# Optimization experiments

Measured on AMD Instinct MI355X. Metric: run time of the kernel, lower is better.

## Reference

```python
import jax, jax.numpy as jnp
import numpy as np


def _greedy_nms_single(scores, suppress):
    """Greedy score-ordered suppression for one scene.
    scores: [P] float max class score; suppress: [P, P] bool, row i suppresses col j
    (same class AND within class radius of point i). Returns keep mask [P] bool."""
    P = scores.shape[0]

    def cond(state):
        alive, _ = state
        return jnp.any(alive)

    def body(state):
        alive, keep = state
        i = jnp.argmax(jnp.where(alive, scores, -jnp.inf))  # highest-score remaining
        keep = keep.at[i].set(True)
        alive = alive & ~suppress[i]   # drop same-class points within radius of i
        alive = alive.at[i].set(False)
        return alive, keep

    alive0 = jnp.ones((P,), dtype=bool)
    keep0 = jnp.zeros((P,), dtype=bool)
    _, keep = jax.lax.while_loop(cond, body, (alive0, keep0))
    return keep


def _keep_mask(centers, cls_preds, class_radius):
    # centers: [B,P,3], cls_preds: [B,P,K], class_radius: [K]
    scores = jnp.max(cls_preds, axis=-1)     # [B,P]  torch.max(..., dim=1) values
    labels = jnp.argmax(cls_preds, axis=-1)  # [B,P]  torch.max(..., dim=1) indices
    diff = centers[:, :, None, :] - centers[:, None, :, :]        # [B,P,P,3]
    dist = jnp.sqrt(jnp.sum(diff * diff, axis=-1))                # [B,P,P] torch.norm
    same_class = labels[:, :, None] == labels[:, None, :]         # [B,P,P]
    radii = class_radius[labels]                                  # [B,P] radius of keeper i
    suppress = same_class & (dist < radii[:, :, None])            # [B,P,P]
    return jax.vmap(_greedy_nms_single)(scores, suppress)         # [B,P] bool


def setup_inputs() -> dict:
    key = jax.random.key(0)
    k1, k2, k3, k4 = jax.random.split(key, 4)
    B, P, C, K = 8, 2048, 1024, 3
    centers = jax.random.normal(k1, (B, P, 3), dtype=jnp.float32)
    features = jax.random.normal(k2, (B, P, C), dtype=jnp.float32)
    cls_preds = jax.random.normal(k3, (B, P, K), dtype=jnp.float32)
    class_radius = jax.random.uniform(k4, (K,), dtype=jnp.float32)  # per-class NMS radius
    return {"centers": centers, "features": features, "cls_preds": cls_preds,
            "class_radius": class_radius}


def reference(centers, features, cls_preds, class_radius):
    """Greedy per-class radius-based keypoint suppression (fixed-shape variant):
    instead of dynamically gathering kept points (data-dependent shape), we return
    the boolean keep mask and the inputs with suppressed entries zeroed out."""
    keep = _keep_mask(centers, cls_preds, class_radius)      # [B,P] bool
    m = keep[..., None].astype(features.dtype)
    return (centers * m, features * m, cls_preds * m, keep)
```

## Files before the change

kernel.cpp:

```cpp
#include <hip/hip_runtime.h>

#define B 8
#define P 2048
#define C 1024
#define NCHUNK 32
#define FEAT4 (B*P*C/4)
#define CEN4  (B*P*3/4)

typedef unsigned long long u64;
typedef unsigned int u32;

__global__ __launch_bounds__(512) void rank_kernel(
    const float* __restrict__ centers,
    const float* __restrict__ cls_preds,
    float4* __restrict__ scent,
    int* __restrict__ sidx)
{
    __shared__ u64 s_keys[P];
    __shared__ u32 s_cnt[64][9];
    const int b = blockIdx.x >> 5, gi = blockIdx.x & 31;
    const int tid = threadIdx.x, wv = tid >> 6, lane = tid & 63;
    const float* clsb = cls_preds + (size_t)b * P * 3;
    const float* cenb = centers + (size_t)b * P * 3;

    for (int e = tid; e < P; e += 512) {
        float s0 = clsb[e*3], s1 = clsb[e*3+1], s2 = clsb[e*3+2];
        float sc = s0; int lb = 0;
        if (s1 > sc) { sc = s1; lb = 1; }
        if (s2 > sc) { sc = s2; lb = 2; }
        u32 ub = __float_as_uint(sc);
        u32 ord = (ub & 0x80000000u) ? ~ub : (ub | 0x80000000u);
        s_keys[e] = ((u64)(~ord) << 32) | (u32)((e << 2) | lb);
    }
    __syncthreads();

    const u64 myk = s_keys[(gi << 6) + lane];
    u32 c = 0;
    const int sbase = wv << 8;
    #pragma unroll 8
    for (int u = 0; u < 256; ++u)
        c += (s_keys[sbase + u] < myk) ? 1u : 0u;
    s_cnt[lane][wv] = c;
    __syncthreads();

    if (wv == 0) {
        u32 rank = 0;
        #pragma unroll
        for (int s = 0; s < 8; ++s) rank += s_cnt[lane][s];
        u32 lo = (u32)myk;
        int orig = (int)(lo >> 2);
        float4 cc;
        cc.x = cenb[orig*3]; cc.y = cenb[orig*3+1]; cc.z = cenb[orig*3+2];
        cc.w = __int_as_float((int)(lo & 3));
        scent[(size_t)b * P + rank] = cc;
        sidx[(size_t)b * P + rank] = (int)lo;
    }
}

__global__ __launch_bounds__(512) void matrix_kernel(
    const float4* __restrict__ scent,
    const float* __restrict__ class_radius,
    u32* __restrict__ matT)
{
    __shared__ float4 s_cent[P];
    const int b = blockIdx.x >> 5, gi = blockIdx.x & 31;
    const int tid = threadIdx.x, wv = tid >> 6, lane = tid & 63;

    const float4 cj = scent[(size_t)b * P + (gi << 6) + lane];
    const int labj = __float_as_int(cj.w);
    const float r = class_radius[labj];
    const float r2 = r * r;
    const int wmin = gi << 1;

    for (int i = tid; i < P; i += 512) s_cent[i] = scent[(size_t)b * P + i];
    __syncthreads();

    for (int w = wv; w < 64; w += 8) {
        if (w < wmin) continue;
        u32 acc = 0;
        #pragma unroll
        for (int u = 0; u < 32; ++u) {
            float4 ci = s_cent[(w << 5) + u];
            float dx = cj.x - ci.x, dy = cj.y - ci.y, dz = cj.z - ci.z;
            bool sup = (__float_as_int(ci.w) == labj)
                       && (dx*dx + dy*dy + dz*dz < r2);
            acc |= ((u32)sup) << u;
        }
        matT[((size_t)b * 64 + w) * P + (gi << 6) + lane] = acc;
    }
}

__global__ __launch_bounds__(576) void scan_kernel(
    const u32* __restrict__ matT,
    const int* __restrict__ sidx,
    float* __restrict__ out_keep)
{
    __shared__ int s_sidx[P];
    __shared__ u32 s_removed[64];
    __shared__ u64 s_keepm[NCHUNK];
    const int b = blockIdx.x;
    const int tid = threadIdx.x, wv = tid >> 6, lane = tid & 63;
    const u32* mb = matT + (size_t)b * 64 * P;

    for (int i = tid; i < P; i += 576) s_sidx[i] = sidx[(size_t)b * P + i];
    if (tid < 64) s_removed[tid] = 0;

    uint4 Va[4], Vb[4];
    u32 Ra[4], Rb[4];
    const int qb = (wv - 1) << 3;

    #pragma unroll
    for (int c = 0; c < 3; ++c) {
        if (wv >= 1) {
            const u32* p = mb + (size_t)lane * P + (c << 6) + qb;
            Va[c] = *(const uint4*)p;
            Vb[c] = *(const uint4*)(p + 4);
        } else {
            Ra[c] = mb[(size_t)(2*c    ) * P + (c << 6) + lane];
            Rb[c] = mb[(size_t)(2*c + 1) * P + (c << 6) + lane];
        }
    }
    __syncthreads();

    #pragma unroll
    for (int g = 0; g < NCHUNK; ++g) {
        const int slot = g & 3;
        if (g + 3 < NCHUNK) {
            const int c = g + 3, ns = c & 3;
            if (wv >= 1) {
                const u32* p = mb + (size_t)lane * P + (c << 6) + qb;
                Va[ns] = *(const uint4*)p;
                Vb[ns] = *(const uint4*)(p + 4);
            } else {
                Ra[ns] = mb[(size_t)(2*c    ) * P + (c << 6) + lane];
                Rb[ns] = mb[(size_t)(2*c + 1) * P + (c << 6) + lane];
            }
        }
        if (wv == 0) {
            u64 row = (u64)Ra[slot] | ((u64)Rb[slot] << 32);
            u64 rem = (u64)s_removed[2*g] | ((u64)s_removed[2*g + 1] << 32);
            u64 alive = ~rem;
            const u64 below = (1ull << lane) - 1ull;
            u64 keepm = 0;
            while (alive) {
                bool ok = ((alive >> lane) & 1ull) && ((row & alive & below) == 0ull);
                u64 newk = __ballot(ok);
                keepm |= newk;
                bool dead = (row & newk) != 0ull;
                u64 deadm = __ballot(dead);
                alive &= ~(newk | deadm);
            }
            if (lane == 0) s_keepm[g] = keepm;
        }
        __syncthreads();
        if (wv >= 1) {
            const u32 kb = (u32)(s_keepm[g] >> qb) & 0xffu;
            u32 acc = 0;
            if (kb & 0x01u) acc |= Va[slot].x;
            if (kb & 0x02u) acc |= Va[slot].y;
            if (kb & 0x04u) acc |= Va[slot].z;
            if (kb & 0x08u) acc |= Va[slot].w;
            if (kb & 0x10u) acc |= Vb[slot].x;
            if (kb & 0x20u) acc |= Vb[slot].y;
            if (kb & 0x40u) acc |= Vb[slot].z;
            if (kb & 0x80u) acc |= Vb[slot].w;
            if (acc) atomicOr(&s_removed[lane], acc);
        }
        __syncthreads();
    }

    for (int pos = tid; pos < P; pos += 576) {
        u64 km = s_keepm[pos >> 6];
        int orig = s_sidx[pos] >> 2;
        out_keep[(size_t)b * P + orig] = ((km >> (pos & 63)) & 1ull) ? 1.0f : 0.0f;
    }
}

__global__ __launch_bounds__(256) void mask_kernel(
    const float* __restrict__ centers,
    const float* __restrict__ features,
    const float* __restrict__ cls_preds,
    const float* __restrict__ keep,
    float* __restrict__ out_centers,
    float* __restrict__ out_feat,
    float* __restrict__ out_cls)
{
    const int idx = blockIdx.x * 256 + threadIdx.x;
    if (idx < FEAT4) {
        const int row = idx >> 8;
        const float m = keep[row];
        if (m != 0.0f) {
            float4 v = ((const float4*)features)[idx];
            v.x *= m; v.y *= m; v.z *= m; v.w *= m;
            ((float4*)out_feat)[idx] = v;
        } else {
            float4 z; z.x = 0.f; z.y = 0.f; z.z = 0.f; z.w = 0.f;
            ((float4*)out_feat)[idx] = z;
        }
    } else if (idx < FEAT4 + CEN4) {
        const int q = idx - FEAT4;
        float4 v = ((const float4*)centers)[q];
        const int e = q * 4;
        v.x *= keep[(e    ) / 3]; v.y *= keep[(e + 1) / 3];
        v.z *= keep[(e + 2) / 3]; v.w *= keep[(e + 3) / 3];
        ((float4*)out_centers)[q] = v;
    } else if (idx < FEAT4 + 2 * CEN4) {
        const int q = idx - FEAT4 - CEN4;
        float4 v = ((const float4*)cls_preds)[q];
        const int e = q * 4;
        v.x *= keep[(e    ) / 3]; v.y *= keep[(e + 1) / 3];
        v.z *= keep[(e + 2) / 3]; v.w *= keep[(e + 3) / 3];
        ((float4*)out_cls)[q] = v;
    }
}

extern "C" void kernel_launch(void* const* d_in, const int* in_sizes, int n_in,
                              void* d_out, int out_size, void* d_ws, size_t ws_size,
                              hipStream_t stream) {
    const float* centers      = (const float*)d_in[0];
    const float* features     = (const float*)d_in[1];
    const float* cls_preds    = (const float*)d_in[2];
    const float* class_radius = (const float*)d_in[3];

    float* out = (float*)d_out;
    float* out_centers = out;
    float* out_feat    = out + (size_t)B * P * 3;
    float* out_cls     = out_feat + (size_t)B * P * C;
    float* out_keep    = out_cls + (size_t)B * P * 3;

    u32*    matT  = (u32*)out_feat;
    float4* scent = (float4*)(out_feat + 1048576);
    int*    sidx  = (int*)(out_feat + 1048576 + 65536);

    hipLaunchKernelGGL(rank_kernel, dim3(B * 32), dim3(512), 0, stream,
                       centers, cls_preds, scent, sidx);
    hipLaunchKernelGGL(matrix_kernel, dim3(B * 32), dim3(512), 0, stream,
                       scent, class_radius, matT);
    hipLaunchKernelGGL(scan_kernel, dim3(B), dim3(576), 0, stream,
                       matT, sidx, out_keep);
    hipLaunchKernelGGL(mask_kernel, dim3((FEAT4 + 2 * CEN4 + 255) / 256), dim3(256),
                       0, stream,
                       centers, features, cls_preds, out_keep,
                       out_centers, out_feat, out_cls);
}
```

Baseline: 171.3 us.

## Pipeline NMS scan by carrying next-chunk suppression in wave 0

```diff
diff --git a/kernel.cpp b/kernel.cpp
--- a/kernel.cpp
+++ b/kernel.cpp
@@ -70,7 +70,7 @@
     const int labj = __float_as_int(cj.w);
     const float r = class_radius[labj];
     const float r2 = r * r;
-    const int wmin = gi << 1;
+    const int wmin = (gi << 1) - 2;
 
     for (int i = tid; i < P; i += 512) s_cent[i] = scent[(size_t)b * P + i];
     __syncthreads();
@@ -106,7 +106,7 @@
     if (tid < 64) s_removed[tid] = 0;
 
     uint4 Va[4], Vb[4];
-    u32 Ra[4], Rb[4];
+    u32 Da[4], Db[4], Na[4], Nb[4];
     const int qb = (wv - 1) << 3;
 
     #pragma unroll
@@ -116,30 +116,25 @@
             Va[c] = *(const uint4*)p;
             Vb[c] = *(const uint4*)(p + 4);
         } else {
-            Ra[c] = mb[(size_t)(2*c    ) * P + (c << 6) + lane];
-            Rb[c] = mb[(size_t)(2*c + 1) * P + (c << 6) + lane];
-        }
-    }
-    __syncthreads();
+            Da[c] = mb[(size_t)(2*c    ) * P + (c << 6) + lane];
+            Db[c] = mb[(size_t)(2*c + 1) * P + (c << 6) + lane];
+            Na[c] = mb[(size_t)(2*c    ) * P + ((c + 1) << 6) + lane];
+            Nb[c] = mb[(size_t)(2*c + 1) * P + ((c + 1) << 6) + lane];
+        }
+    }
+    asm volatile("s_waitcnt lgkmcnt(0)" ::: "memory");
+    __builtin_amdgcn_s_barrier();
+
+    u32 carrybit = 0;
 
     #pragma unroll
     for (int g = 0; g < NCHUNK; ++g) {
         const int slot = g & 3;
-        if (g + 3 < NCHUNK) {
-            const int c = g + 3, ns = c & 3;
-            if (wv >= 1) {
-                const u32* p = mb + (size_t)lane * P + (c << 6) + qb;
-                Va[ns] = *(const uint4*)p;
-                Vb[ns] = *(const uint4*)(p + 4);
-            } else {
-                Ra[ns] = mb[(size_t)(2*c    ) * P + (c << 6) + lane];
-                Rb[ns] = mb[(size_t)(2*c + 1) * P + (c << 6) + lane];
-            }
-        }
         if (wv == 0) {
-            u64 row = (u64)Ra[slot] | ((u64)Rb[slot] << 32);
             u64 rem = (u64)s_removed[2*g] | ((u64)s_removed[2*g + 1] << 32);
-            u64 alive = ~rem;
+            u64 carrym = __ballot(carrybit != 0u);
+            u64 alive = ~(rem | carrym);
+            u64 row = (u64)Da[slot] | ((u64)Db[slot] << 32);
             const u64 below = (1ull << lane) - 1ull;
             u64 keepm = 0;
             while (alive) {
@@ -151,22 +146,41 @@
                 alive &= ~(newk | deadm);
             }
             if (lane == 0) s_keepm[g] = keepm;
-        }
-        __syncthreads();
-        if (wv >= 1) {
-            const u32 kb = (u32)(s_keepm[g] >> qb) & 0xffu;
-            u32 acc = 0;
-            if (kb & 0x01u) acc |= Va[slot].x;
-            if (kb & 0x02u) acc |= Va[slot].y;
-            if (kb & 0x04u) acc |= Va[slot].z;
-            if (kb & 0x08u) acc |= Va[slot].w;
-            if (kb & 0x10u) acc |= Vb[slot].x;
-            if (kb & 0x20u) acc |= Vb[slot].y;
-            if (kb & 0x40u) acc |= Vb[slot].z;
-            if (kb & 0x80u) acc |= Vb[slot].w;
-            if (acc) atomicOr(&s_removed[lane], acc);
-        }
-        __syncthreads();
+            if (g + 1 < NCHUNK)
+                carrybit = (Na[slot] & (u32)keepm) | (Nb[slot] & (u32)(keepm >> 32));
+            if (g + 3 < NCHUNK) {
+                const int cc = g + 3, ns = cc & 3;
+                Da[ns] = mb[(size_t)(2*cc    ) * P + (cc << 6) + lane];
+                Db[ns] = mb[(size_t)(2*cc + 1) * P + (cc << 6) + lane];
+                if (cc + 1 < NCHUNK) {
+                    Na[ns] = mb[(size_t)(2*cc    ) * P + ((cc + 1) << 6) + lane];
+                    Nb[ns] = mb[(size_t)(2*cc + 1) * P + ((cc + 1) << 6) + lane];
+                }
+            }
+        } else {
+            if (g >= 1) {
+                const int ps = (g - 1) & 3;
+                const u32 kb = (u32)(s_keepm[g - 1] >> qb) & 0xffu;
+                u32 acc = 0;
+                if (kb & 0x01u) acc |= Va[ps].x;
+                if (kb & 0x02u) acc |= Va[ps].y;
+                if (kb & 0x04u) acc |= Va[ps].z;
+                if (kb & 0x08u) acc |= Va[ps].w;
+                if (kb & 0x10u) acc |= Vb[ps].x;
+                if (kb & 0x20u) acc |= Vb[ps].y;
+                if (kb & 0x40u) acc |= Vb[ps].z;
+                if (kb & 0x80u) acc |= Vb[ps].w;
+                if (acc) atomicOr(&s_removed[lane], acc);
+            }
+            if (g + 3 < NCHUNK - 1) {
+                const int cc = g + 3, ns = cc & 3;
+                const u32* p = mb + (size_t)lane * P + (cc << 6) + qb;
+                Va[ns] = *(const uint4*)p;
+                Vb[ns] = *(const uint4*)(p + 4);
+            }
+        }
+        asm volatile("s_waitcnt lgkmcnt(0)" ::: "memory");
+        __builtin_amdgcn_s_barrier();
     }
 
     for (int pos = tid; pos < P; pos += 576) {
```

After: 159.4 us. 6.9% less time.

## Process NMS chunks in pairs with register carries to halve scan barriers

Applied to the files above, without the earlier changes.

```diff
diff --git a/kernel.cpp b/kernel.cpp
--- a/kernel.cpp
+++ b/kernel.cpp
@@ -4,6 +4,7 @@
 #define P 2048
 #define C 1024
 #define NCHUNK 32
+#define NGRP 16
 #define FEAT4 (B*P*C/4)
 #define CEN4  (B*P*3/4)
 
@@ -70,7 +71,7 @@
     const int labj = __float_as_int(cj.w);
     const float r = class_radius[labj];
     const float r2 = r * r;
-    const int wmin = gi << 1;
+    const int wmin = (gi << 1) - 6;
 
     for (int i = tid; i < P; i += 512) s_cent[i] = scent[(size_t)b * P + i];
     __syncthreads();
@@ -88,6 +89,20 @@
         }
         matT[((size_t)b * 64 + w) * P + (gi << 6) + lane] = acc;
     }
+}
+
+__device__ __forceinline__ u64 peel64(u64 alive, u64 row, int lane) {
+    const u64 below = (1ull << lane) - 1ull;
+    u64 keepm = 0;
+    while (alive) {
+        bool ok = ((alive >> lane) & 1ull) && ((row & alive & below) == 0ull);
+        u64 newk = __ballot(ok);
+        keepm |= newk;
+        bool dead = (row & newk) != 0ull;
+        u64 deadm = __ballot(dead);
+        alive &= ~(newk | deadm);
+    }
+    return keepm;
 }
 
 __global__ __launch_bounds__(576) void scan_kernel(
@@ -106,67 +121,124 @@
     if (tid < 64) s_removed[tid] = 0;
 
     uint4 Va[4], Vb[4];
-    u32 Ra[4], Rb[4];
+    u32 Daa[4], Dab[4], Dba[4], Dbb[4];
+    u32 N1a[4], N1b[4], N2a[4], N2b[4], N3a[4], N3b[4];
+    u32 N4a[4], N4b[4], N5a[4], N5b[4];
     const int qb = (wv - 1) << 3;
 
-    #pragma unroll
-    for (int c = 0; c < 3; ++c) {
-        if (wv >= 1) {
+    if (wv >= 1) {
+        #pragma unroll
+        for (int c = 0; c < 2; ++c) {
             const u32* p = mb + (size_t)lane * P + (c << 6) + qb;
             Va[c] = *(const uint4*)p;
             Vb[c] = *(const uint4*)(p + 4);
+        }
+    } else {
+        #pragma unroll
+        for (int t = 0; t < 3; ++t) {
+            const int a = 2*t, bb = 2*t + 1;
+            Daa[t] = mb[(size_t)(2*a   ) * P + (a  << 6) + lane];
+            Dab[t] = mb[(size_t)(2*a + 1) * P + (a  << 6) + lane];
+            Dba[t] = mb[(size_t)(2*bb   ) * P + (bb << 6) + lane];
+            Dbb[t] = mb[(size_t)(2*bb + 1) * P + (bb << 6) + lane];
+            N1a[t] = mb[(size_t)(2*a   ) * P + (bb << 6) + lane];
+            N1b[t] = mb[(size_t)(2*a + 1) * P + (bb << 6) + lane];
+            N2a[t] = mb[(size_t)(2*a   ) * P + ((a + 2) << 6) + lane];
+            N2b[t] = mb[(size_t)(2*a + 1) * P + ((a + 2) << 6) + lane];
+            N4a[t] = mb[(size_t)(2*bb   ) * P + ((a + 2) << 6) + lane];
+            N4b[t] = mb[(size_t)(2*bb + 1) * P + ((a + 2) << 6) + lane];
+            N3a[t] = mb[(size_t)(2*a   ) * P + ((a + 3) << 6) + lane];
+            N3b[t] = mb[(size_t)(2*a + 1) * P + ((a + 3) << 6) + lane];
+            N5a[t] = mb[(size_t)(2*bb   ) * P + ((a + 3) << 6) + lane];
+            N5b[t] = mb[(size_t)(2*bb + 1) * P + ((a + 3) << 6) + lane];
+        }
+    }
+    asm volatile("s_waitcnt lgkmcnt(0)" ::: "memory");
+    __builtin_amdgcn_s_barrier();
+
+    u32 carryA = 0, carryB = 0;
+
+    #pragma unroll
+    for (int t = 0; t < NGRP; ++t) {
+        const int slot = t & 3;
+        if (wv == 0) {
+            const u32 r0 = s_removed[4*t    ], r1 = s_removed[4*t + 1];
+            const u32 r2 = s_removed[4*t + 2], r3 = s_removed[4*t + 3];
+            u64 carrymA = __ballot(carryA != 0u);
+            u64 aliveA = ~(((u64)r0 | ((u64)r1 << 32)) | carrymA);
+            u64 rowA = (u64)Daa[slot] | ((u64)Dab[slot] << 32);
+            u64 keepA = peel64(aliveA, rowA, lane);
+            if (lane == 0) s_keepm[2*t] = keepA;
+            const u32 cab = (N1a[slot] & (u32)keepA) | (N1b[slot] & (u32)(keepA >> 32));
+            u64 carrymB = __ballot((carryB | cab) != 0u);
+            u64 aliveB = ~(((u64)r2 | ((u64)r3 << 32)) | carrymB);
+            u64 rowB = (u64)Dba[slot] | ((u64)Dbb[slot] << 32);
+            u64 keepB = peel64(aliveB, rowB, lane);
+            if (lane == 0) s_keepm[2*t + 1] = keepB;
+            if (t + 1 < NGRP) {
+                carryA = (N2a[slot] & (u32)keepA) | (N2b[slot] & (u32)(keepA >> 32))
+                       | (N4a[slot] & (u32)keepB) | (N4b[slot] & (u32)(keepB >> 32));
+                carryB = (N3a[slot] & (u32)keepA) | (N3b[slot] & (u32)(keepA >> 32))
+                       | (N5a[slot] & (u32)keepB) | (N5b[slot] & (u32)(keepB >> 32));
+            }
+            if (t + 3 < NGRP) {
+                const int tt = t + 3, ns = tt & 3;
+                const int a = 2*tt, bb = 2*tt + 1;
+                Daa[ns] = mb[(size_t)(2*a   ) * P + (a  << 6) + lane];
+                Dab[ns] = mb[(size_t)(2*a + 1) * P + (a  << 6) + lane];
+                Dba[ns] = mb[(size_t)(2*bb   ) * P + (bb << 6) + lane];
+                Dbb[ns] = mb[(size_t)(2*bb + 1) * P + (bb << 6) + lane];
+                N1a[ns] = mb[(size_t)(2*a   ) * P + (bb << 6) + lane];
+                N1b[ns] = mb[(size_t)(2*a + 1) * P + (bb << 6) + lane];
+                if (a + 2 < NCHUNK) {
+                    N2a[ns] = mb[(size_t)(2*a   ) * P + ((a + 2) << 6) + lane];
+                    N2b[ns] = mb[(size_t)(2*a + 1) * P + ((a + 2) << 6) + lane];
+                    N4a[ns] = mb[(size_t)(2*bb   ) * P + ((a + 2) << 6) + lane];
+                    N4b[ns] = mb[(size_t)(2*bb + 1) * P + ((a + 2) << 6) + lane];
+                }
+                if (a + 3 < NCHUNK) {
+                    N3a[ns] = mb[(size_t)(2*a   ) * P + ((a + 3) << 6) + lane];
+                    N3b[ns] = mb[(size_t)(2*a + 1) * P + ((a + 3) << 6) + lane];
+                    N5a[ns] = mb[(size_t)(2*bb   ) * P + ((a + 3) << 6) + lane];
+                    N5b[ns] = mb[(size_t)(2*bb + 1) * P + ((a + 3) << 6) + lane];
+                }
+            }
         } else {
-            Ra[c] = mb[(size_t)(2*c    ) * P + (c << 6) + lane];
-            Rb[c] = mb[(size_t)(2*c + 1) * P + (c << 6) + lane];
-        }
-    }
-    __syncthreads();
-
-    #pragma unroll
-    for (int g = 0; g < NCHUNK; ++g) {
-        const int slot = g & 3;
-        if (g + 3 < NCHUNK) {
-            const int c = g + 3, ns = c & 3;
-            if (wv >= 1) {
-                const u32* p = mb + (size_t)lane * P + (c << 6) + qb;
-                Va[ns] = *(const uint4*)p;
-                Vb[ns] = *(const uint4*)(p + 4);
-            } else {
-                Ra[ns] = mb[(size_t)(2*c    ) * P + (c << 6) + lane];
-                Rb[ns] = mb[(size_t)(2*c + 1) * P + (c << 6) + lane];
+            if (t >= 1) {
+                const int pa = (2*t - 2) & 3, pb = (2*t - 1) & 3;
+                const u32 kb0 = (u32)(s_keepm[2*t - 2] >> qb) & 0xffu;
+                const u32 kb1 = (u32)(s_keepm[2*t - 1] >> qb) & 0xffu;
+                u32 acc = 0;
+                if (kb0 & 0x01u) acc |= Va[pa].x;
+                if (kb0 & 0x02u) acc |= Va[pa].y;
+                if (kb0 & 0x04u) acc |= Va[pa].z;
+                if (kb0 & 0x08u) acc |= Va[pa].w;
+                if (kb0 & 0x10u) acc |= Vb[pa].x;
+                if (kb0 & 0x20u) acc |= Vb[pa].y;
+                if (kb0 & 0x40u) acc |= Vb[pa].z;
+                if (kb0 & 0x80u) acc |= Vb[pa].w;
+                if (kb1 & 0x01u) acc |= Va[pb].x;
+                if (kb1 & 0x02u) acc |= Va[pb].y;
+                if (kb1 & 0x04u) acc |= Va[pb].z;
+                if (kb1 & 0x08u) acc |= Va[pb].w;
+                if (kb1 & 0x10u) acc |= Vb[pb].x;
+                if (kb1 & 0x20u) acc |= Vb[pb].y;
+                if (kb1 & 0x40u) acc |= Vb[pb].z;
+                if (kb1 & 0x80u) acc |= Vb[pb].w;
+                if (acc) atomicOr(&s_removed[lane], acc);
             }
-        }
-        if (wv == 0) {
-            u64 row = (u64)Ra[slot] | ((u64)Rb[slot] << 32);
-            u64 rem = (u64)s_removed[2*g] | ((u64)s_removed[2*g + 1] << 32);
-            u64 alive = ~rem;
-            const u64 below = (1ull << lane) - 1ull;
-            u64 keepm = 0;
-            while (alive) {
-                bool ok = ((alive >> lane) & 1ull) && ((row & alive & below) == 0ull);
-                u64 newk = __ballot(ok);
-                keepm |= newk;
-                bool dead = (row & newk) != 0ull;
-                u64 deadm = __ballot(dead);
-                alive &= ~(newk | deadm);
+            if (t + 1 < NGRP - 1) {
+                const int c0 = 2*t + 2, c1 = 2*t + 3;
+                const u32* p0 = mb + (size_t)lane * P + (c0 << 6) + qb;
+                const u32* p1 = mb + (size_t)lane * P + (c1 << 6) + qb;
+                Va[c0 & 3] = *(const uint4*)p0;
+                Vb[c0 & 3] = *(const uint4*)(p0 + 4);
+                Va[c1 & 3] = *(const uint4*)p1;
+                Vb[c1 & 3] = *(const uint4*)(p1 + 4);
             }
-            if (lane == 0) s_keepm[g] = keepm;
-        }
-        __syncthreads();
-        if (wv >= 1) {
-            const u32 kb = (u32)(s_keepm[g] >> qb) & 0xffu;
-            u32 acc = 0;
-            if (kb & 0x01u) acc |= Va[slot].x;
-            if (kb & 0x02u) acc |= Va[slot].y;
-            if (kb & 0x04u) acc |= Va[slot].z;
-            if (kb & 0x08u) acc |= Va[slot].w;
-            if (kb & 0x10u) acc |= Vb[slot].x;
-            if (kb & 0x20u) acc |= Vb[slot].y;
-            if (kb & 0x40u) acc |= Vb[slot].z;
-            if (kb & 0x80u) acc |= Vb[slot].w;
-            if (acc) atomicOr(&s_removed[lane], acc);
-        }
-        __syncthreads();
+        }
+        asm volatile("s_waitcnt lgkmcnt(0)" ::: "memory");
+        __builtin_amdgcn_s_barrier();
     }
 
     for (int pos = tid; pos < P; pos += 576) {
```

Measured after the change: 158.5 us. 1.08x faster.

## Rewrite NMS scan as single-wavefront register-resident pass with 64-bit row layout

Applied to the files above, without the earlier changes.

```diff
diff --git a/kernel.cpp b/kernel.cpp
--- a/kernel.cpp
+++ b/kernel.cpp
@@ -60,7 +60,7 @@
 __global__ __launch_bounds__(512) void matrix_kernel(
     const float4* __restrict__ scent,
     const float* __restrict__ class_radius,
-    u32* __restrict__ matT)
+    u64* __restrict__ matI)
 {
     __shared__ float4 s_cent[P];
     const int b = blockIdx.x >> 5, gi = blockIdx.x & 31;
@@ -70,110 +70,95 @@
     const int labj = __float_as_int(cj.w);
     const float r = class_radius[labj];
     const float r2 = r * r;
-    const int wmin = gi << 1;
 
     for (int i = tid; i < P; i += 512) s_cent[i] = scent[(size_t)b * P + i];
     __syncthreads();
 
-    for (int w = wv; w < 64; w += 8) {
-        if (w < wmin) continue;
-        u32 acc = 0;
+    for (int p = wv; p < 32; p += 8) {
+        u32 lo = 0, hi = 0;
         #pragma unroll
         for (int u = 0; u < 32; ++u) {
-            float4 ci = s_cent[(w << 5) + u];
+            float4 ci = s_cent[(p << 6) + u];
             float dx = cj.x - ci.x, dy = cj.y - ci.y, dz = cj.z - ci.z;
             bool sup = (__float_as_int(ci.w) == labj)
                        && (dx*dx + dy*dy + dz*dz < r2);
-            acc |= ((u32)sup) << u;
+            lo |= ((u32)sup) << u;
         }
-        matT[((size_t)b * 64 + w) * P + (gi << 6) + lane] = acc;
-    }
-}
-
-__global__ __launch_bounds__(576) void scan_kernel(
-    const u32* __restrict__ matT,
+        #pragma unroll
+        for (int u = 0; u < 32; ++u) {
+            float4 ci = s_cent[(p << 6) + 32 + u];
+            float dx = cj.x - ci.x, dy = cj.y - ci.y, dz = cj.z - ci.z;
+            bool sup = (__float_as_int(ci.w) == labj)
+                       && (dx*dx + dy*dy + dz*dz < r2);
+            hi |= ((u32)sup) << u;
+        }
+        matI[((size_t)b * 32 + p) * P + (gi << 6) + lane]
+            = (u64)lo | ((u64)hi << 32);
+    }
+}
+
+#define PROCESS(BK, DG, g)                                                   \
+  {                                                                          \
+    u64 alive = ~__ballot(((supp >> (g)) & 1u) != 0u);                       \
+    const u64 row = (DG);                                                    \
+    u64 keepm = 0;                                                           \
+    while (alive) {                         \
+      bool okk = ((alive >> lane) & 1ull) && ((row & alive & below) == 0ull);\
+      u64 newk = __ballot(okk);                                              \
+      keepm |= newk;                                                         \
+      bool dead = (row & newk) != 0ull;                                      \
+      u64 deadm = __ballot(dead);                                            \
+      alive &= ~(newk | deadm);                                              \
+    }                                                                        \
+    keepbits |= ((u32)((keepm >> lane) & 1ull)) << (g);                      \
+    u32 nb = 0;                                                              \
+    _Pragma("unroll")                                                        \
+    for (int h = 0; h < 32; ++h)                                             \
+      nb |= ((BK[h] & keepm) != 0ull ? 1u : 0u) << h;                        \
+    supp |= nb & (u32)~((2ull << (g)) - 1ull);       \
+  }
+
+#define RELOAD(BK, DG, g)                                                    \
+  {                                                                          \
+    const u64* pp = mbI + (size_t)(g) * P + lane;                            \
+    _Pragma("unroll")                                                        \
+    for (int h = 0; h < 32; ++h) BK[h] = pp[h * 64];                         \
+    (DG) = pp[(g) * 64];                                                     \
+  }
+
+__global__ __launch_bounds__(64, 1) void scan_kernel(
+    const u64* __restrict__ matI,
     const int* __restrict__ sidx,
     float* __restrict__ out_keep)
 {
-    __shared__ int s_sidx[P];
-    __shared__ u32 s_removed[64];
-    __shared__ u64 s_keepm[NCHUNK];
     const int b = blockIdx.x;
-    const int tid = threadIdx.x, wv = tid >> 6, lane = tid & 63;
-    const u32* mb = matT + (size_t)b * 64 * P;
-
-    for (int i = tid; i < P; i += 576) s_sidx[i] = sidx[(size_t)b * P + i];
-    if (tid < 64) s_removed[tid] = 0;
-
-    uint4 Va[4], Vb[4];
-    u32 Ra[4], Rb[4];
-    const int qb = (wv - 1) << 3;
-
+    const int lane = threadIdx.x;
+    const u64* mbI = matI + (size_t)b * 32 * P;
+    const u64 below = (1ull << lane) - 1ull;
+
+    u64 bank0[32], bank1[32];
+    u64 d0, d1;
+    u32 supp = 0, keepbits = 0;
+
+    RELOAD(bank0, d0, 0);
+    RELOAD(bank1, d1, 1);
+
+    for (int t = 0; t < NCHUNK / 2; ++t) {
+        const int g = 2 * t;
+        PROCESS(bank0, d0, g);
+        if (t < NCHUNK / 2 - 1) RELOAD(bank0, d0, g + 2);
+        PROCESS(bank1, d1, g + 1);
+        if (t < NCHUNK / 2 - 1) RELOAD(bank1, d1, g + 3);
+    }
+
+    const int* sp = sidx + (size_t)b * P;
+    int sv[32];
     #pragma unroll
-    for (int c = 0; c < 3; ++c) {
-        if (wv >= 1) {
-            const u32* p = mb + (size_t)lane * P + (c << 6) + qb;
-            Va[c] = *(const uint4*)p;
-            Vb[c] = *(const uint4*)(p + 4);
-        } else {
-            Ra[c] = mb[(size_t)(2*c    ) * P + (c << 6) + lane];
-            Rb[c] = mb[(size_t)(2*c + 1) * P + (c << 6) + lane];
-        }
-    }
-    __syncthreads();
-
+    for (int h = 0; h < 32; ++h) sv[h] = sp[h * 64 + lane];
+    float* okp = out_keep + (size_t)b * P;
     #pragma unroll
-    for (int g = 0; g < NCHUNK; ++g) {
-        const int slot = g & 3;
-        if (g + 3 < NCHUNK) {
-            const int c = g + 3, ns = c & 3;
-            if (wv >= 1) {
-                const u32* p = mb + (size_t)lane * P + (c << 6) + qb;
-                Va[ns] = *(const uint4*)p;
-                Vb[ns] = *(const uint4*)(p + 4);
-            } else {
-                Ra[ns] = mb[(size_t)(2*c    ) * P + (c << 6) + lane];
-                Rb[ns] = mb[(size_t)(2*c + 1) * P + (c << 6) + lane];
-            }
-        }
-        if (wv == 0) {
-            u64 row = (u64)Ra[slot] | ((u64)Rb[slot] << 32);
-            u64 rem = (u64)s_removed[2*g] | ((u64)s_removed[2*g + 1] << 32);
-            u64 alive = ~rem;
-            const u64 below = (1ull << lane) - 1ull;
-            u64 keepm = 0;
-            while (alive) {
-                bool ok = ((alive >> lane) & 1ull) && ((row & alive & below) == 0ull);
-                u64 newk = __ballot(ok);
-                keepm |= newk;
-                bool dead = (row & newk) != 0ull;
-                u64 deadm = __ballot(dead);
-                alive &= ~(newk | deadm);
-            }
-            if (lane == 0) s_keepm[g] = keepm;
-        }
-        __syncthreads();
-        if (wv >= 1) {
-            const u32 kb = (u32)(s_keepm[g] >> qb) & 0xffu;
-            u32 acc = 0;
-            if (kb & 0x01u) acc |= Va[slot].x;
-            if (kb & 0x02u) acc |= Va[slot].y;
-            if (kb & 0x04u) acc |= Va[slot].z;
-            if (kb & 0x08u) acc |= Va[slot].w;
-            if (kb & 0x10u) acc |= Vb[slot].x;
-            if (kb & 0x20u) acc |= Vb[slot].y;
-            if (kb & 0x40u) acc |= Vb[slot].z;
-            if (kb & 0x80u) acc |= Vb[slot].w;
-            if (acc) atomicOr(&s_removed[lane], acc);
-        }
-        __syncthreads();
-    }
-
-    for (int pos = tid; pos < P; pos += 576) {
-        u64 km = s_keepm[pos >> 6];
-        int orig = s_sidx[pos] >> 2;
-        out_keep[(size_t)b * P + orig] = ((km >> (pos & 63)) & 1ull) ? 1.0f : 0.0f;
-    }
+    for (int h = 0; h < 32; ++h)
+        okp[sv[h] >> 2] = ((keepbits >> h) & 1u) ? 1.0f : 0.0f;
 }
 
 __global__ __launch_bounds__(256) void mask_kernel(
@@ -228,16 +213,16 @@
     float* out_cls     = out_feat + (size_t)B * P * C;
     float* out_keep    = out_cls + (size_t)B * P * 3;
 
-    u32*    matT  = (u32*)out_feat;
+    u64*    matI  = (u64*)out_feat;
     float4* scent = (float4*)(out_feat + 1048576);
     int*    sidx  = (int*)(out_feat + 1048576 + 65536);
 
     hipLaunchKernelGGL(rank_kernel, dim3(B * 32), dim3(512), 0, stream,
                        centers, cls_preds, scent, sidx);
     hipLaunchKernelGGL(matrix_kernel, dim3(B * 32), dim3(512), 0, stream,
-                       scent, class_radius, matT);
-    hipLaunchKernelGGL(scan_kernel, dim3(B), dim3(576), 0, stream,
-                       matT, sidx, out_keep);
+                       scent, class_radius, matI);
+    hipLaunchKernelGGL(scan_kernel, dim3(B), dim3(64), 0, stream,
+                       matI, sidx, out_keep);
     hipLaunchKernelGGL(mask_kernel, dim3((FEAT4 + 2 * CEN4 + 255) / 256), dim3(256),
                        0, stream,
                        centers, features, cls_preds, out_keep,
```

Result: faster. 163.4 us (-4.6%).
